# Kernel optimization log

Measured on AMD Instinct MI355X. Metric: run time of the kernel, lower is better.

Reference implementation:

```python
import jax, jax.numpy as jnp
import numpy as np

# ---- piecewise-linear surrogate tables (constants of the surrogate ops) ----
_N = 512
_GX = np.linspace(-10.0, 10.0, _N).astype(np.float32)
_GY = (0.5 * _GX * (1.0 + np.tanh(np.sqrt(2.0 / np.pi) * (_GX + 0.044715 * _GX ** 3)))).astype(np.float32)
_EX = np.linspace(-30.0, 0.0, _N).astype(np.float32)
_EY = np.exp(_EX).astype(np.float32)
_IX = np.geomspace(1e-3, 4096.0, _N).astype(np.float32)
_IY = (1.0 / _IX).astype(np.float32)
_RX = np.geomspace(1e-6, 100.0, _N).astype(np.float32)
_RY = (1.0 / np.sqrt(_RX)).astype(np.float32)

GX, GY = jnp.asarray(_GX), jnp.asarray(_GY)
EX, EY = jnp.asarray(_EX), jnp.asarray(_EY)
IX, IY = jnp.asarray(_IX), jnp.asarray(_IY)
RX, RY = jnp.asarray(_RX), jnp.asarray(_RY)

EXP_CLIP_MIN = -30.0
LN_EPS = 1e-5
N_HEAD = 16

pwl_gelu = lambda x: jnp.interp(x, GX, GY)
pwl_exp = lambda x: jnp.interp(x, EX, EY)
pwl_inv = lambda x: jnp.interp(x, IX, IY)
pwl_rsqrt = lambda x: jnp.interp(x, RX, RY)


def _layernorm_approx(x, w, b):
    mu = jnp.mean(x, axis=-1, keepdims=True)
    xc = x - mu
    var = jnp.mean(xc * xc, axis=-1, keepdims=True)
    inv_std = pwl_rsqrt(var + LN_EPS)
    return xc * inv_std * w + b


def _attn_approx(x, c_attn_w, c_attn_b, c_proj_w, c_proj_b):
    B, T, D = x.shape
    hd = D // N_HEAD
    scale = 1.0 / jnp.sqrt(jnp.float32(hd))
    qkv = x @ c_attn_w + c_attn_b                      # [B,T,3D]
    q, k, v = jnp.split(qkv, 3, axis=-1)
    q = q.reshape(B, T, N_HEAD, hd).transpose(0, 2, 1, 3)  # [B,H,T,hd]
    k = k.reshape(B, T, N_HEAD, hd).transpose(0, 2, 1, 3)
    v = v.reshape(B, T, N_HEAD, hd).transpose(0, 2, 1, 3)
    scores = jnp.einsum('bhqd,bhkd->bhqk', q, k) * scale    # [B,H,T,T]
    causal = jnp.tril(jnp.ones((T, T), dtype=bool))
    scores = jnp.where(causal, scores, -jnp.inf)
    m = jnp.max(scores, axis=-1, keepdims=True)
    s = jnp.clip(scores - m, EXP_CLIP_MIN, 0.0)             # masked -> -30
    e = pwl_exp(s)
    p = e * pwl_inv(jnp.sum(e, axis=-1, keepdims=True))
    out = jnp.einsum('bhqk,bhkd->bhqd', p, v)
    out = out.transpose(0, 2, 1, 3).reshape(B, T, D)
    return out @ c_proj_w + c_proj_b


def _mlp_approx(x, fc_w, fc_b, proj_w, proj_b):
    h = pwl_gelu(x @ fc_w + fc_b)
    return h @ proj_w + proj_b


def setup_inputs() -> dict:
    key = jax.random.key(0)
    ks = jax.random.split(key, 8)
    B, T, D = 2, 1024, 2048
    DF = 4 * D
    w = 0.02
    return {
        'x': jax.random.normal(ks[0], (B, T, D), jnp.float32),
        'ln_1_w': jnp.ones((D,), jnp.float32),
        'ln_1_b': jnp.zeros((D,), jnp.float32),
        'ln_2_w': jnp.ones((D,), jnp.float32),
        'ln_2_b': jnp.zeros((D,), jnp.float32),
        'c_attn_w': w * jax.random.normal(ks[1], (D, 3 * D), jnp.float32),
        'c_attn_b': jnp.zeros((3 * D,), jnp.float32),
        'c_proj_w': w * jax.random.normal(ks[2], (D, D), jnp.float32),
        'c_proj_b': jnp.zeros((D,), jnp.float32),
        'fc_w': w * jax.random.normal(ks[3], (D, DF), jnp.float32),
        'fc_b': jnp.zeros((DF,), jnp.float32),
        'proj_w': w * jax.random.normal(ks[4], (DF, D), jnp.float32),
        'proj_b': jnp.zeros((D,), jnp.float32),
    }


def reference(x, ln_1_w, ln_1_b, ln_2_w, ln_2_b, c_attn_w, c_attn_b,
              c_proj_w, c_proj_b, fc_w, fc_b, proj_w, proj_b):
    x = x + _attn_approx(_layernorm_approx(x, ln_1_w, ln_1_b),
                         c_attn_w, c_attn_b, c_proj_w, c_proj_b)
    x = x + _mlp_approx(_layernorm_approx(x, ln_2_w, ln_2_b),
                        fc_w, fc_b, proj_w, proj_b)
    return x
```

## Files before the change

kernel.cpp:

```cpp
#include <hip/hip_runtime.h>
#include <hip/hip_bf16.h>
#include <stdint.h>

typedef unsigned short u16;
typedef __bf16 bf16x8 __attribute__((ext_vector_type(8)));
typedef float f32x4 __attribute__((ext_vector_type(4)));
typedef u16 u16x8 __attribute__((ext_vector_type(8)));

#define MFMA16(a, b, c) __builtin_amdgcn_mfma_f32_16x16x32_bf16(a, b, c, 0, 0, 0)

typedef __attribute__((address_space(3))) unsigned as3_uint;
typedef __attribute__((address_space(1))) unsigned as1_uint;

__device__ __forceinline__ void gload_lds16(const void* g, void* l) {
  __builtin_amdgcn_global_load_lds((const as1_uint*)g, (as3_uint*)l, 16, 0, 0);
}

__device__ __forceinline__ u16 f2bf(float f) {
  unsigned u = __float_as_uint(f);
  u += 0x7FFF + ((u >> 16) & 1);
  return (u16)(u >> 16);
}

__device__ __forceinline__ float pwl_lin(float x, float x0, float x1, float invStep,
                                         const float* __restrict__ Bt,
                                         const float* __restrict__ Ct) {
  float xc = fminf(fmaxf(x, x0), x1);
  int i = (int)floorf((x - x0) * invStep);
  i = max(0, min(510, i));
  return fmaf(Bt[i], xc, Ct[i]);
}

__device__ __forceinline__ float pwl_log(float x, float x0, float x1, float lnx0, float invL,
                                         const float* __restrict__ Bt,
                                         const float* __restrict__ Ct) {
  float xc = fminf(fmaxf(x, x0), x1);
  int i = (int)floorf((logf(xc) - lnx0) * invL);
  i = max(0, min(510, i));
  return fmaf(Bt[i], xc, Ct[i]);
}

__global__ void init_tables(float* __restrict__ tb) {
  __shared__ float xs[4][512], ys[4][512];
  int i = threadIdx.x;
  if (i < 512) {
    double t = (double)i / 511.0;
    float xg = (float)(-10.0 + 20.0 * t);
    double xd = (double)xg;
    xs[0][i] = xg;
    ys[0][i] = (float)(0.5 * xd * (1.0 + tanh(0.7978845608028654 * (xd + 0.044715 * xd * xd * xd))));
    float xe = (float)(-30.0 + 30.0 * t);
    xs[1][i] = xe;
    ys[1][i] = (float)exp((double)xe);
    double li = -3.0 + t * (log10(4096.0) + 3.0);
    float xi = (float)pow(10.0, li);
    if (i == 0) xi = 1e-3f;
    if (i == 511) xi = 4096.0f;
    xs[2][i] = xi;
    ys[2][i] = 1.0f / xi;
    double lr = -6.0 + t * 8.0;
    float xr2 = (float)pow(10.0, lr);
    if (i == 0) xr2 = 1e-6f;
    if (i == 511) xr2 = 100.0f;
    xs[3][i] = xr2;
    ys[3][i] = 1.0f / sqrtf(xr2);
  }
  __syncthreads();
  if (i < 511) {
#pragma unroll
    for (int tc = 0; tc < 4; ++tc) {
      double bq = ((double)ys[tc][i + 1] - (double)ys[tc][i]) /
                  ((double)xs[tc][i + 1] - (double)xs[tc][i]);
      double cq = (double)ys[tc][i] - bq * (double)xs[tc][i];
      tb[tc * 1024 + i] = (float)bq;
      tb[tc * 1024 + 512 + i] = (float)cq;
    }
  }
}

__global__ __launch_bounds__(256) void ln_kernel(const float* __restrict__ x,
                                                 const float* __restrict__ w,
                                                 const float* __restrict__ b,
                                                 u16* __restrict__ out,
                                                 const float* __restrict__ tb) {
  int row = blockIdx.x, tid = threadIdx.x;
  const float4* xr = (const float4*)(x + (size_t)row * 2048);
  float4 v0 = xr[tid], v1 = xr[tid + 256];
  float s = ((v0.x + v0.y) + (v0.z + v0.w)) + ((v1.x + v1.y) + (v1.z + v1.w));
#pragma unroll
  for (int m = 32; m; m >>= 1) s += __shfl_xor(s, m, 64);
  __shared__ float red1[4], red2[4];
  int wv = tid >> 6;
  if ((tid & 63) == 0) red1[wv] = s;
  __syncthreads();
  float mu = (red1[0] + red1[1] + red1[2] + red1[3]) * (1.0f / 2048.0f);
  float a0 = v0.x - mu, a1 = v0.y - mu, a2 = v0.z - mu, a3 = v0.w - mu;
  float a4 = v1.x - mu, a5 = v1.y - mu, a6 = v1.z - mu, a7 = v1.w - mu;
  float q = ((a0 * a0 + a1 * a1) + (a2 * a2 + a3 * a3)) +
            ((a4 * a4 + a5 * a5) + (a6 * a6 + a7 * a7));
#pragma unroll
  for (int m = 32; m; m >>= 1) q += __shfl_xor(q, m, 64);
  if ((tid & 63) == 0) red2[wv] = q;
  __syncthreads();
  float var = (red2[0] + red2[1] + red2[2] + red2[3]) * (1.0f / 2048.0f);
  float istd = pwl_log(var + 1e-5f, 1e-6f, 100.0f, -13.8155106f, 27.7405655f, tb + 3072, tb + 3584);
  const float4* wr4 = (const float4*)w;
  const float4* br4 = (const float4*)b;
  float4 w0 = wr4[tid], w1 = wr4[tid + 256];
  float4 b0 = br4[tid], b1 = br4[tid + 256];
  u16 o0 = f2bf(fmaf(a0 * istd, w0.x, b0.x));
  u16 o1 = f2bf(fmaf(a1 * istd, w0.y, b0.y));
  u16 o2 = f2bf(fmaf(a2 * istd, w0.z, b0.z));
  u16 o3 = f2bf(fmaf(a3 * istd, w0.w, b0.w));
  u16 o4 = f2bf(fmaf(a4 * istd, w1.x, b1.x));
  u16 o5 = f2bf(fmaf(a5 * istd, w1.y, b1.y));
  u16 o6 = f2bf(fmaf(a6 * istd, w1.z, b1.z));
  u16 o7 = f2bf(fmaf(a7 * istd, w1.w, b1.w));
  uint2 p0, p1;
  p0.x = (unsigned)o0 | ((unsigned)o1 << 16);
  p0.y = (unsigned)o2 | ((unsigned)o3 << 16);
  p1.x = (unsigned)o4 | ((unsigned)o5 << 16);
  p1.y = (unsigned)o6 | ((unsigned)o7 << 16);
  uint2* orow = (uint2*)(out + (size_t)row * 2048);
  orow[tid] = p0;
  orow[tid + 256] = p1;
}

__global__ __launch_bounds__(256) void cast_transpose(const float* __restrict__ W,
                                                      u16* __restrict__ WT, int K, int N) {
  __shared__ u16 s[64][130];
  int j0 = blockIdx.x * 64, i0 = blockIdx.y * 128;
  int tid = threadIdx.x;
  int c = tid & 63, g = tid >> 6;
#pragma unroll
  for (int rr = g; rr < 128; rr += 4) {
    s[c][rr] = f2bf(W[(size_t)(i0 + rr) * N + j0 + c]);
  }
  __syncthreads();
  int r = tid >> 2;
  int cc0 = (tid & 3) * 32;
  unsigned* dst = (unsigned*)(WT + (size_t)(j0 + r) * K + i0 + cc0);
#pragma unroll
  for (int ii = 0; ii < 16; ++ii) {
    unsigned lo = s[r][cc0 + 2 * ii], hi = s[r][cc0 + 2 * ii + 1];
    dst[ii] = lo | (hi << 16);
  }
}

__global__ __launch_bounds__(256) void vtrans_kernel(const u16* __restrict__ qkv,
                                                     u16* __restrict__ vt) {
  int tt = blockIdx.x, dd = blockIdx.y, bh = blockIdx.z;
  int b = bh >> 4, h = bh & 15;
  __shared__ u16 s[64][72];
  int tid = threadIdx.x;
  const u16* src = qkv + ((size_t)b * 1024 + tt * 64) * 6144 + 4096 + h * 128 + dd * 64;
#pragma unroll
  for (int it = 0; it < 2; ++it) {
    int idx = it * 256 + tid;
    int r = idx >> 3, c = idx & 7;
    u16x8 v = *(const u16x8*)(src + (size_t)r * 6144 + c * 8);
#pragma unroll
    for (int j = 0; j < 8; ++j) s[r][c * 8 + j] = v[j];
  }
  __syncthreads();
  u16* dst = vt + ((size_t)bh * 128 + dd * 64) * 1024 + tt * 64;
#pragma unroll
  for (int it = 0; it < 2; ++it) {
    int idx = it * 256 + tid;
    int d = idx >> 3, c2 = idx & 7;
    u16x8 o;
#pragma unroll
    for (int j = 0; j < 8; ++j) o[j] = s[c2 * 8 + j][d];
    *(u16x8*)(dst + (size_t)d * 1024 + c2 * 8) = o;
  }
}

template <int EPI>
__global__ __launch_bounds__(256) void gemm_bt(const u16* __restrict__ A,
                                               const u16* __restrict__ BT,
                                               const float* __restrict__ bias,
                                               const float* __restrict__ add,
                                               float* __restrict__ outF,
                                               u16* __restrict__ outH, int M, int N, int K,
                                               const float* __restrict__ tb) {
  __shared__ u16 sA[128 * 32], sB[128 * 32];
  int tid = threadIdx.x, lane = tid & 63, w = tid >> 6;
  int l15 = lane & 15, lg = lane >> 4;
  int wr = w >> 1, wc = w & 1;
  int mBase = blockIdx.y * 128, nBase = blockIdx.x * 128;

  f32x4 acc[4][4] = {};

  int rowA = tid >> 2, chA = tid & 3;
  const u16* gA = A + (size_t)(mBase + rowA) * K + chA * 8;
  const u16* gB = BT + (size_t)(nBase + rowA) * K + chA * 8;
  u16* sAw = sA + w * 512;
  u16* sAw2 = sA + 2048 + w * 512;
  u16* sBw = sB + w * 512;
  u16* sBw2 = sB + 2048 + w * 512;
  size_t k64 = (size_t)64 * K;

  for (int k0 = 0; k0 < K; k0 += 32) {
    gload_lds16(gA + k0, sAw);
    gload_lds16(gA + k0 + k64, sAw2);
    gload_lds16(gB + k0, sBw);
    gload_lds16(gB + k0 + k64, sBw2);
    __syncthreads();
    bf16x8 aF[4], bF[4];
#pragma unroll
    for (int m = 0; m < 4; ++m)
      aF[m] = *(const bf16x8*)&sA[(wr * 64 + m * 16 + l15) * 32 + lg * 8];
#pragma unroll
    for (int n = 0; n < 4; ++n)
      bF[n] = *(const bf16x8*)&sB[(wc * 64 + n * 16 + l15) * 32 + lg * 8];
#pragma unroll
    for (int m = 0; m < 4; ++m)
#pragma unroll
      for (int n = 0; n < 4; ++n) acc[m][n] = MFMA16(aF[m], bF[n], acc[m][n]);
    __syncthreads();
  }

  float bv[4];
#pragma unroll
  for (int n = 0; n < 4; ++n) bv[n] = bias[nBase + wc * 64 + n * 16 + l15];
#pragma unroll
  for (int m = 0; m < 4; ++m) {
    int row0 = mBase + wr * 64 + m * 16 + lg * 4;
#pragma unroll
    for (int n = 0; n < 4; ++n) {
      int col = nBase + wc * 64 + n * 16 + l15;
#pragma unroll
      for (int r = 0; r < 4; ++r) {
        size_t oidx = (size_t)(row0 + r) * N + col;
        float v = acc[m][n][r] + bv[n];
        if (EPI == 1) {
          v += add[oidx];
          outF[oidx] = v;
        } else if (EPI == 2) {
          v = pwl_lin(v, -10.0f, 10.0f, 511.0f / 20.0f, tb, tb + 512);
          outH[oidx] = f2bf(v);
        } else {
          outH[oidx] = f2bf(v);
        }
      }
    }
  }
}

template <int EPI>
__global__ __launch_bounds__(512) void gemm_bt_sk(const u16* __restrict__ A,
                                                  const u16* __restrict__ BT,
                                                  const float* __restrict__ bias,
                                                  const float* __restrict__ add,
                                                  float* __restrict__ outF,
                                                  u16* __restrict__ outH, int M, int N, int K,
                                                  const float* __restrict__ tb) {
  __shared__ u16 smem[16384];
  u16* sA = smem;
  u16* sB = smem + 8192;
  float* red = (float*)smem;

  int tid = threadIdx.x, lane = tid & 63, w = tid >> 6;
  int l15 = lane & 15, lg = lane >> 4;
  int q = w & 3, grp = w >> 2;
  int wr = q >> 1, wc = q & 1;
  int mBase = blockIdx.y * 128, nBase = blockIdx.x * 128;
  int Kh = K >> 1;

  f32x4 acc[4][4] = {};

  int ts = tid & 255;
  int rowA = ts >> 2, chA = ts & 3;
  const u16* gA = A + (size_t)(mBase + rowA) * K + (size_t)grp * Kh + chA * 8;
  const u16* gB = BT + (size_t)(nBase + rowA) * K + (size_t)grp * Kh + chA * 8;
  int w4 = w & 3;
  u16* sAw = sA + grp * 4096 + w4 * 512;
  u16* sAw2 = sA + grp * 4096 + 2048 + w4 * 512;
  u16* sBw = sB + grp * 4096 + w4 * 512;
  u16* sBw2 = sB + grp * 4096 + 2048 + w4 * 512;
  size_t k64 = (size_t)64 * K;
  const u16* sAr = sA + grp * 4096;
  const u16* sBr = sB + grp * 4096;

  for (int k0 = 0; k0 < Kh; k0 += 32) {
    gload_lds16(gA + k0, sAw);
    gload_lds16(gA + k0 + k64, sAw2);
    gload_lds16(gB + k0, sBw);
    gload_lds16(gB + k0 + k64, sBw2);
    __syncthreads();
    bf16x8 aF[4], bF[4];
#pragma unroll
    for (int m = 0; m < 4; ++m)
      aF[m] = *(const bf16x8*)&sAr[(wr * 64 + m * 16 + l15) * 32 + lg * 8];
#pragma unroll
    for (int n = 0; n < 4; ++n)
      bF[n] = *(const bf16x8*)&sBr[(wc * 64 + n * 16 + l15) * 32 + lg * 8];
#pragma unroll
    for (int m = 0; m < 4; ++m)
#pragma unroll
      for (int n = 0; n < 4; ++n) acc[m][n] = MFMA16(aF[m], bF[n], acc[m][n]);
    __syncthreads();
  }

  float bv[4];
#pragma unroll
  for (int n = 0; n < 4; ++n) bv[n] = bias[nBase + wc * 64 + n * 16 + l15];

#pragma unroll
  for (int chunk = 0; chunk < 2; ++chunk) {
    if (grp == 1) {
#pragma unroll
      for (int mm = 0; mm < 2; ++mm)
#pragma unroll
        for (int n = 0; n < 4; ++n)
          *(f32x4*)(red + ((q * 8 + mm * 4 + n) << 8) + lane * 4) = acc[chunk * 2 + mm][n];
    }
    __syncthreads();
    if (grp == 0) {
#pragma unroll
      for (int mm = 0; mm < 2; ++mm) {
        int m = chunk * 2 + mm;
        int row0 = mBase + wr * 64 + m * 16 + lg * 4;
#pragma unroll
        for (int n = 0; n < 4; ++n) {
          f32x4 o = *(const f32x4*)(red + ((q * 8 + mm * 4 + n) << 8) + lane * 4);
          f32x4 a = acc[m][n];
          int col = nBase + wc * 64 + n * 16 + l15;
#pragma unroll
          for (int r = 0; r < 4; ++r) {
            size_t oidx = (size_t)(row0 + r) * N + col;
            float v = a[r] + o[r] + bv[n];
            if (EPI == 1) {
              v += add[oidx];
              outF[oidx] = v;
            } else if (EPI == 2) {
              v = pwl_lin(v, -10.0f, 10.0f, 511.0f / 20.0f, tb, tb + 512);
              outH[oidx] = f2bf(v);
            } else {
              outH[oidx] = f2bf(v);
            }
          }
        }
      }
    }
    __syncthreads();
  }
}

__global__ __launch_bounds__(256) void attn_kernel(const u16* __restrict__ qkv,
                                                   const u16* __restrict__ vt,
                                                   u16* __restrict__ outA,
                                                   const float* __restrict__ tb) {
  int bid = blockIdx.x;
  int qt = 15 - (bid >> 5);
  int bh = bid & 31;
  int b = bh >> 4, h = bh & 15;
  int tid = threadIdx.x, lane = tid & 63, w = tid >> 6;
  int l15 = lane & 15, lg = lane >> 4;

  __shared__ u16 sQ[64 * 128];
  __shared__ u16 sK[64 * 128];
  __shared__ u16 sVT[128 * 64];
  __shared__ __bf16 sP[4][16 * 72];

  const size_t RS = 6144;
  int q0 = qt * 64;
  const u16* qg = qkv + ((size_t)b * 1024 + q0) * RS + h * 128;
  const u16* kg = qkv + (size_t)b * 1024 * RS + 2048 + h * 128;
  const u16* vg = vt + (size_t)bh * 128 * 1024;
  int ntiles = qt + 1;
  const float scale = 0.08838834764831845f;
  const float* EB = tb + 1024;
  const float* EC = tb + 1536;

#pragma unroll
  for (int it = 0; it < 4; ++it) {
    int idx = it * 256 + tid;
    int r = idx >> 4, ch = idx & 15;
    gload_lds16(qg + (size_t)r * RS + (ch ^ (r & 7)) * 8, sQ + (size_t)(it * 256 + w * 64) * 8);
  }
  __syncthreads();

  bf16x8 aQ[4];
#pragma unroll
  for (int kk = 0; kk < 4; ++kk) {
    int row = w * 16 + l15;
    int off = (row * 256 + ((kk * 64 + lg * 16) ^ ((row & 7) << 4))) >> 1;
    aQ[kk] = *(const bf16x8*)&sQ[off];
  }

  float mrun[4], ssum[4];
#pragma unroll
  for (int r = 0; r < 4; ++r) {
    mrun[r] = -3.0e38f;
    ssum[r] = 0.f;
  }
  f32x4 oacc[8] = {};
  int qrow_w = q0 + w * 16;

  for (int t = 0; t < ntiles; ++t) {
    __syncthreads();
#pragma unroll
    for (int it = 0; it < 4; ++it) {
      int idx = it * 256 + tid;
      int r = idx >> 4, ch = idx & 15;
      gload_lds16(kg + (size_t)(t * 64 + r) * RS + (ch ^ (r & 7)) * 8,
                  sK + (size_t)(it * 256 + w * 64) * 8);
      int d = idx >> 3, c = idx & 7;
      gload_lds16(vg + (size_t)d * 1024 + t * 64 + (c ^ (d & 7)) * 8,
                  sVT + (size_t)(it * 256 + w * 64) * 8);
    }
    __syncthreads();

    f32x4 sc[4];
#pragma unroll
    for (int n = 0; n < 4; ++n) {
      sc[n] = (f32x4){0.f, 0.f, 0.f, 0.f};
#pragma unroll
      for (int kk = 0; kk < 4; ++kk) {
        int row = n * 16 + l15;
        int off = (row * 256 + ((kk * 64 + lg * 16) ^ ((row & 7) << 4))) >> 1;
        bf16x8 bK = *(const bf16x8*)&sK[off];
        sc[n] = MFMA16(aQ[kk], bK, sc[n]);
      }
    }

    float mt[4], sv[4][4];
#pragma unroll
    for (int r = 0; r < 4; ++r) mt[r] = -3.0e38f;
#pragma unroll
    for (int n = 0; n < 4; ++n)
#pragma unroll
      for (int r = 0; r < 4; ++r) {
        int key = t * 64 + n * 16 + l15;
        int qq = qrow_w + lg * 4 + r;
        float v = (key <= qq) ? sc[n][r] * scale : -3.0e38f;
        sv[n][r] = v;
        mt[r] = fmaxf(mt[r], v);
      }
#pragma unroll
    for (int m = 8; m; m >>= 1)
#pragma unroll
      for (int r = 0; r < 4; ++r) mt[r] = fmaxf(mt[r], __shfl_xor(mt[r], m, 64));

#pragma unroll
    for (int r = 0; r < 4; ++r) {
      float mn = fmaxf(mrun[r], mt[r]);
      float f = __expf(mrun[r] - mn);
      mrun[r] = mn;
      ssum[r] *= f;
#pragma unroll
      for (int fi = 0; fi < 8; ++fi) oacc[fi][r] *= f;
    }

#pragma unroll
    for (int n = 0; n < 4; ++n)
#pragma unroll
      for (int r = 0; r < 4; ++r) {
        float scv = fminf(fmaxf(sv[n][r] - mrun[r], -30.0f), 0.0f);
        float e = pwl_lin(scv, -30.0f, 0.0f, 511.0f / 30.0f, EB, EC);
        ssum[r] += e;
        sP[w][(lg * 4 + r) * 72 + n * 16 + l15] = (__bf16)e;
      }

#pragma unroll
    for (int kk = 0; kk < 2; ++kk) {
      bf16x8 aP = *(const bf16x8*)&sP[w][l15 * 72 + kk * 32 + lg * 8];
#pragma unroll
      for (int fi = 0; fi < 8; ++fi) {
        int d = fi * 16 + l15;
        int off = (d * 128 + ((kk * 64 + lg * 16) ^ ((d & 7) << 4))) >> 1;
        bf16x8 bV = *(const bf16x8*)&sVT[off];
        oacc[fi] = MFMA16(aP, bV, oacc[fi]);
      }
    }
  }

#pragma unroll
  for (int m = 8; m; m >>= 1)
#pragma unroll
    for (int r = 0; r < 4; ++r) ssum[r] += __shfl_xor(ssum[r], m, 64);

  int skipped = 1024 - ntiles * 64;
#pragma unroll
  for (int r = 0; r < 4; ++r) {
    float s = ssum[r] + (float)skipped * 9.357623e-14f;
    float inv = pwl_log(s, 1e-3f, 4096.0f, -6.9077553f, 33.5620689f, tb + 2048, tb + 2560);
    int qq = qrow_w + lg * 4 + r;
    size_t base = ((size_t)b * 1024 + qq) * 2048 + (size_t)h * 128;
#pragma unroll
    for (int fi = 0; fi < 8; ++fi) outA[base + fi * 16 + l15] = f2bf(oacc[fi][r] * inv);
  }
}

extern "C" void kernel_launch(void* const* d_in, const int* in_sizes, int n_in, void* d_out,
                              int out_size, void* d_ws, size_t ws_size, hipStream_t stream) {
  const float* x = (const float*)d_in[0];
  const float* ln1w = (const float*)d_in[1];
  const float* ln1b = (const float*)d_in[2];
  const float* ln2w = (const float*)d_in[3];
  const float* ln2b = (const float*)d_in[4];
  const float* attnW = (const float*)d_in[5];
  const float* attnB = (const float*)d_in[6];
  const float* projW = (const float*)d_in[7];
  const float* projB = (const float*)d_in[8];
  const float* fcW = (const float*)d_in[9];
  const float* fcB = (const float*)d_in[10];
  const float* proj2W = (const float*)d_in[11];
  const float* proj2B = (const float*)d_in[12];
  float* out = (float*)d_out;

  char* ws = (char*)d_ws;
  float* tb = (float*)ws;
  u16* WT = (u16*)(ws + 16384);
  u16* VT = WT;
  u16* ABUF = (u16*)(ws + 16384 + 33554432);
  u16* QBUF = (u16*)(ws + 16384 + 33554432 + 8388608);
  float* X1 = (float*)(ws + 16384 + 33554432 + 8388608 + 33554432);

  init_tables<<<1, 512, 0, stream>>>(tb);

  ln_kernel<<<2048, 256, 0, stream>>>(x, ln1w, ln1b, ABUF, tb);
  cast_transpose<<<dim3(6144 / 64, 2048 / 128), 256, 0, stream>>>(attnW, WT, 2048, 6144);
  gemm_bt<0><<<dim3(48, 16), 256, 0, stream>>>(ABUF, WT, attnB, nullptr, nullptr, QBUF, 2048,
                                               6144, 2048, tb);
  vtrans_kernel<<<dim3(16, 2, 32), 256, 0, stream>>>(QBUF, VT);
  attn_kernel<<<512, 256, 0, stream>>>(QBUF, VT, ABUF, tb);
  cast_transpose<<<dim3(2048 / 64, 2048 / 128), 256, 0, stream>>>(projW, WT, 2048, 2048);
  gemm_bt_sk<1><<<dim3(16, 16), 512, 0, stream>>>(ABUF, WT, projB, x, X1, nullptr, 2048, 2048,
                                                  2048, tb);
  ln_kernel<<<2048, 256, 0, stream>>>(X1, ln2w, ln2b, ABUF, tb);
  cast_transpose<<<dim3(8192 / 64, 2048 / 128), 256, 0, stream>>>(fcW, WT, 2048, 8192);
  gemm_bt<2><<<dim3(64, 16), 256, 0, stream>>>(ABUF, WT, fcB, nullptr, nullptr, QBUF, 2048,
                                               8192, 2048, tb);
  cast_transpose<<<dim3(2048 / 64, 8192 / 128), 256, 0, stream>>>(proj2W, WT, 8192, 2048);
  gemm_bt_sk<1><<<dim3(16, 16), 512, 0, stream>>>(QBUF, WT, proj2B, X1, out, nullptr, 2048,
                                                  2048, 8192, tb);
}
```

Measured before the change: 702.6 us.

## Double-buffer LDS in split-K GEMM to overlap global loads with MFMA

```diff
diff --git a/kernel.cpp b/kernel.cpp
--- a/kernel.cpp
+++ b/kernel.cpp
@@ -255,9 +255,7 @@
                                                   float* __restrict__ outF,
                                                   u16* __restrict__ outH, int M, int N, int K,
                                                   const float* __restrict__ tb) {
-  __shared__ u16 smem[16384];
-  u16* sA = smem;
-  u16* sB = smem + 8192;
+  __shared__ u16 smem[32768];
   float* red = (float*)smem;
 
   int tid = threadIdx.x, lane = tid & 63, w = tid >> 6;
@@ -266,6 +264,7 @@
   int wr = q >> 1, wc = q & 1;
   int mBase = blockIdx.y * 128, nBase = blockIdx.x * 128;
   int Kh = K >> 1;
+  int NT = Kh >> 5;
 
   f32x4 acc[4][4] = {};
 
@@ -273,33 +272,46 @@
   int rowA = ts >> 2, chA = ts & 3;
   const u16* gA = A + (size_t)(mBase + rowA) * K + (size_t)grp * Kh + chA * 8;
   const u16* gB = BT + (size_t)(nBase + rowA) * K + (size_t)grp * Kh + chA * 8;
+  size_t k64 = (size_t)64 * K;
   int w4 = w & 3;
-  u16* sAw = sA + grp * 4096 + w4 * 512;
-  u16* sAw2 = sA + grp * 4096 + 2048 + w4 * 512;
-  u16* sBw = sB + grp * 4096 + w4 * 512;
-  u16* sBw2 = sB + grp * 4096 + 2048 + w4 * 512;
-  size_t k64 = (size_t)64 * K;
-  const u16* sAr = sA + grp * 4096;
-  const u16* sBr = sB + grp * 4096;
-
-  for (int k0 = 0; k0 < Kh; k0 += 32) {
-    gload_lds16(gA + k0, sAw);
-    gload_lds16(gA + k0 + k64, sAw2);
-    gload_lds16(gB + k0, sBw);
-    gload_lds16(gB + k0 + k64, sBw2);
-    __syncthreads();
+
+  u16* base = smem + grp * 16384;
+  u16* sAw[2] = {base + w4 * 512, base + 8192 + w4 * 512};
+  u16* sBw[2] = {base + 4096 + w4 * 512, base + 8192 + 4096 + w4 * 512};
+  const u16* sAr[2] = {base, base + 8192};
+  const u16* sBr[2] = {base + 4096, base + 8192 + 4096};
+
+#define STAGE_SK(c, k0)                          \
+  {                                              \
+    gload_lds16(gA + (k0), sAw[c]);              \
+    gload_lds16(gA + (k0) + k64, sAw[c] + 2048); \
+    gload_lds16(gB + (k0), sBw[c]);              \
+    gload_lds16(gB + (k0) + k64, sBw[c] + 2048); \
+  }
+
+  STAGE_SK(0, 0);
+  asm volatile("s_waitcnt vmcnt(0)" ::: "memory");
+  __builtin_amdgcn_s_barrier();
+
+  int cur = 0;
+  for (int t = 0; t < NT; ++t) {
+    if (t + 1 < NT) STAGE_SK(cur ^ 1, (t + 1) * 32);
     bf16x8 aF[4], bF[4];
 #pragma unroll
     for (int m = 0; m < 4; ++m)
-      aF[m] = *(const bf16x8*)&sAr[(wr * 64 + m * 16 + l15) * 32 + lg * 8];
+      aF[m] = *(const bf16x8*)&sAr[cur][(wr * 64 + m * 16 + l15) * 32 + lg * 8];
 #pragma unroll
     for (int n = 0; n < 4; ++n)
-      bF[n] = *(const bf16x8*)&sBr[(wc * 64 + n * 16 + l15) * 32 + lg * 8];
+      bF[n] = *(const bf16x8*)&sBr[cur][(wc * 64 + n * 16 + l15) * 32 + lg * 8];
+    __builtin_amdgcn_s_setprio(1);
 #pragma unroll
     for (int m = 0; m < 4; ++m)
 #pragma unroll
       for (int n = 0; n < 4; ++n) acc[m][n] = MFMA16(aF[m], bF[n], acc[m][n]);
-    __syncthreads();
+    __builtin_amdgcn_s_setprio(0);
+    asm volatile("s_waitcnt vmcnt(0)" ::: "memory");
+    __builtin_amdgcn_s_barrier();
+    cur ^= 1;
   }
 
   float bv[4];
@@ -345,6 +357,7 @@
     }
     __syncthreads();
   }
+#undef STAGE_SK
 }
 
 __global__ __launch_bounds__(256) void attn_kernel(const u16* __restrict__ qkv,
```

New measurement: 711.9 us. No clear change (+1.3%).
